# Kernel tuning notes

Hardware: AMD Instinct MI355X
Metric: run time of the kernel (lower is better)

The kernel has to match this reference:

```python
import jax, jax.numpy as jnp
import numpy as np

D = H = W = 128
NUM_STEPS = 7  # MONAI DVF2DDF default


def _base_grid(dtype):
    zz, yy, xx = jnp.meshgrid(jnp.arange(D, dtype=dtype),
                              jnp.arange(H, dtype=dtype),
                              jnp.arange(W, dtype=dtype), indexing='ij')
    return jnp.stack([zz, yy, xx], 0)  # [3,D,H,W] voxel coords


def _warp(img, ddf, mode):
    # img: [1,C,D,H,W], ddf: [1,3,D,H,W] in voxel units.
    # Equivalent to grid_sample(align_corners=True, padding='border'):
    # border padding == clamp the voxel-space sample coordinate to [0, dim-1].
    dtype = ddf.dtype
    coords = _base_grid(dtype) + ddf[0]
    lims = jnp.array([D - 1, H - 1, W - 1], dtype=dtype).reshape(3, 1, 1, 1)
    coords = jnp.clip(coords, 0.0, lims)
    vol = img[0]  # [C,D,H,W]
    if mode == 'nearest':
        zi, yi, xi = jnp.round(coords).astype(jnp.int32)
        return vol[:, zi, yi, xi][None]
    z, y, x = coords
    z0 = jnp.floor(z); y0 = jnp.floor(y); x0 = jnp.floor(x)
    wz = z - z0; wy = y - y0; wx = x - x0
    z0i = z0.astype(jnp.int32); y0i = y0.astype(jnp.int32); x0i = x0.astype(jnp.int32)
    z1i = jnp.minimum(z0i + 1, D - 1)
    y1i = jnp.minimum(y0i + 1, H - 1)
    x1i = jnp.minimum(x0i + 1, W - 1)
    g = lambda a, b, c: vol[:, a, b, c]  # [C,D,H,W] gather
    out = (g(z0i, y0i, x0i) * (1 - wz) * (1 - wy) * (1 - wx)
         + g(z0i, y0i, x1i) * (1 - wz) * (1 - wy) * wx
         + g(z0i, y1i, x0i) * (1 - wz) * wy * (1 - wx)
         + g(z0i, y1i, x1i) * (1 - wz) * wy * wx
         + g(z1i, y0i, x0i) * wz * (1 - wy) * (1 - wx)
         + g(z1i, y0i, x1i) * wz * (1 - wy) * wx
         + g(z1i, y1i, x0i) * wz * wy * (1 - wx)
         + g(z1i, y1i, x1i) * wz * wy * wx)
    return out[None]


def _dvf2ddf(dvf):
    # scaling-and-squaring integration of a stationary velocity field
    ddf = dvf / (2.0 ** NUM_STEPS)
    for _ in range(NUM_STEPS):
        ddf = ddf + _warp(ddf, ddf, 'bilinear')
    return ddf


def setup_inputs() -> dict:
    key = jax.random.key(0)
    k1, k2, k3, k4 = jax.random.split(key, 4)
    dvf = jax.random.normal(k1, (1, 3, D, H, W), dtype=jnp.float32) * 0.5
    moving_image = jax.random.uniform(k2, (1, 1, D, H, W), dtype=jnp.float32)
    fixed_image = jax.random.uniform(k3, (1, 1, D, H, W), dtype=jnp.float32)
    moving_label = jax.random.randint(k4, (1, 1, D, H, W), 0, 4).astype(jnp.float32)
    return {'dvf': dvf, 'moving_image': moving_image,
            'fixed_image': fixed_image, 'moving_label': moving_label}


def reference(dvf, moving_image, fixed_image, moving_label):
    ddf = _dvf2ddf(dvf)
    pred_image = _warp(moving_image, ddf, 'bilinear')
    pred_label = _warp(moving_label, ddf, 'nearest')
    return (ddf, pred_image, pred_label, dvf)
```

## Files before the change

### kernel.cpp

```cpp
#include <hip/hip_runtime.h>

#define DD 128
constexpr int NV = DD * DD * DD;
constexpr float SCALE = 1.0f / 128.0f;

__device__ __forceinline__ float clampc(float v) {
    return fminf(fmaxf(v, 0.0f), (float)(DD - 1));
}

struct Corners {
    int i000, i001, i010, i011, i100, i101, i110, i111;
    float w000, w001, w010, w011, w100, w101, w110, w111;
};

__device__ __forceinline__ Corners corner_setup(float cz, float cy, float cx) {
    float z0f = floorf(cz), y0f = floorf(cy), x0f = floorf(cx);
    float wz = cz - z0f, wy = cy - y0f, wx = cx - x0f;
    int z0 = (int)z0f, y0 = (int)y0f, x0 = (int)x0f;
    int z1 = min(z0 + 1, DD - 1);
    int y1 = min(y0 + 1, DD - 1);
    int x1 = min(x0 + 1, DD - 1);
    float omz = 1.0f - wz, omy = 1.0f - wy, omx = 1.0f - wx;
    int zs0 = z0 << 14, zs1 = z1 << 14;
    int ys0 = y0 << 7,  ys1 = y1 << 7;
    Corners c;
    c.i000 = zs0 + ys0 + x0; c.i001 = zs0 + ys0 + x1;
    c.i010 = zs0 + ys1 + x0; c.i011 = zs0 + ys1 + x1;
    c.i100 = zs1 + ys0 + x0; c.i101 = zs1 + ys0 + x1;
    c.i110 = zs1 + ys1 + x0; c.i111 = zs1 + ys1 + x1;
    c.w000 = omz * omy * omx; c.w001 = omz * omy * wx;
    c.w010 = omz * wy * omx;  c.w011 = omz * wy * wx;
    c.w100 = wz * omy * omx;  c.w101 = wz * omy * wx;
    c.w110 = wz * wy * omx;   c.w111 = wz * wy * wx;
    return c;
}

__device__ __forceinline__ float3 trilerp4(const float4* __restrict__ src,
                                           const Corners& c, float3 base) {
    float4 v000 = src[c.i000], v001 = src[c.i001];
    float4 v010 = src[c.i010], v011 = src[c.i011];
    float4 v100 = src[c.i100], v101 = src[c.i101];
    float4 v110 = src[c.i110], v111 = src[c.i111];
    float3 r;
    r.x = base.x + c.w000*v000.x + c.w001*v001.x + c.w010*v010.x + c.w011*v011.x
                 + c.w100*v100.x + c.w101*v101.x + c.w110*v110.x + c.w111*v111.x;
    r.y = base.y + c.w000*v000.y + c.w001*v001.y + c.w010*v010.y + c.w011*v011.y
                 + c.w100*v100.y + c.w101*v101.y + c.w110*v110.y + c.w111*v111.y;
    r.z = base.z + c.w000*v000.z + c.w001*v001.z + c.w010*v010.z + c.w011*v011.z
                 + c.w100*v100.z + c.w101*v101.z + c.w110*v110.z + c.w111*v111.z;
    return r;
}


__global__ __launch_bounds__(256)
void pack_kernel(const float* __restrict__ dvf, float4* __restrict__ dst) {
    int tid = blockIdx.x * blockDim.x + threadIdx.x;
    float4 v;
    v.x = dvf[tid] * SCALE;
    v.y = dvf[tid + NV] * SCALE;
    v.z = dvf[tid + 2 * NV] * SCALE;
    v.w = 0.0f;
    dst[tid] = v;
}

__global__ __launch_bounds__(256)
void step_pair_kernel(const float4* __restrict__ src, float4* __restrict__ dst) {
    int t = blockIdx.x * blockDim.x + threadIdx.x;
    int x  = t & (DD - 1);
    int y  = (t >> 7) & (DD - 1);
    int zh = t >> 14;
    int z  = zh << 1;

    int idxA = (z << 14) + (y << 7) + x;
    int idxB = idxA + (1 << 14);

    float4 sA = src[idxA];
    float4 sB = src[idxB];

    Corners cA = corner_setup(clampc((float)z + sA.x),
                              clampc((float)y + sA.y),
                              clampc((float)x + sA.z));
    Corners cB = corner_setup(clampc((float)(z + 1) + sB.x),
                              clampc((float)y + sB.y),
                              clampc((float)x + sB.z));

    float3 rA = trilerp4(src, cA, make_float3(sA.x, sA.y, sA.z));
    float3 rB = trilerp4(src, cB, make_float3(sB.x, sB.y, sB.z));

    dst[idxA] = make_float4(rA.x, rA.y, rA.z, 0.0f);
    dst[idxB] = make_float4(rB.x, rB.y, rB.z, 0.0f);
}

__global__ __launch_bounds__(256)
void step7_final4_kernel(const float4* __restrict__ src,
                         const float* __restrict__ mimg,
                         const float* __restrict__ mlab,
                         const float* __restrict__ dvf,
                         float* __restrict__ ddf_out,
                         float* __restrict__ pred_img,
                         float* __restrict__ pred_lab,
                         float* __restrict__ dvf_out) {
    int tid = blockIdx.x * blockDim.x + threadIdx.x;
    int x = tid & (DD - 1);
    int y = (tid >> 7) & (DD - 1);
    int z = tid >> 14;

    float4 s = src[tid];
    float dv0 = dvf[tid], dv1 = dvf[tid + NV], dv2 = dvf[tid + 2 * NV];

    Corners c = corner_setup(clampc((float)z + s.x),
                             clampc((float)y + s.y),
                             clampc((float)x + s.z));
    float3 r = trilerp4(src, c, make_float3(s.x, s.y, s.z));

    ddf_out[tid]          = r.x;
    ddf_out[tid + NV]     = r.y;
    ddf_out[tid + 2 * NV] = r.z;
    dvf_out[tid]          = dv0;
    dvf_out[tid + NV]     = dv1;
    dvf_out[tid + 2 * NV] = dv2;

    float cz = clampc((float)z + r.x);
    float cy = clampc((float)y + r.y);
    float cx = clampc((float)x + r.z);

    {
        Corners g = corner_setup(cz, cy, cx);
        pred_img[tid] = g.w000*mimg[g.i000] + g.w001*mimg[g.i001]
                      + g.w010*mimg[g.i010] + g.w011*mimg[g.i011]
                      + g.w100*mimg[g.i100] + g.w101*mimg[g.i101]
                      + g.w110*mimg[g.i110] + g.w111*mimg[g.i111];
    }
    {
        int zi = (int)rintf(cz);
        int yi = (int)rintf(cy);
        int xi = (int)rintf(cx);
        pred_lab[tid] = mlab[(zi << 14) + (yi << 7) + xi];
    }
}


__device__ __forceinline__ void trilerp3i(const float* __restrict__ src,
                                          const Corners& c,
                                          float& r0, float& r1, float& r2) {
    const float* p000 = src + 3 * c.i000; const float* p001 = src + 3 * c.i001;
    const float* p010 = src + 3 * c.i010; const float* p011 = src + 3 * c.i011;
    const float* p100 = src + 3 * c.i100; const float* p101 = src + 3 * c.i101;
    const float* p110 = src + 3 * c.i110; const float* p111 = src + 3 * c.i111;
    r0 = c.w000*p000[0] + c.w001*p001[0] + c.w010*p010[0] + c.w011*p011[0]
       + c.w100*p100[0] + c.w101*p101[0] + c.w110*p110[0] + c.w111*p111[0];
    r1 = c.w000*p000[1] + c.w001*p001[1] + c.w010*p010[1] + c.w011*p011[1]
       + c.w100*p100[1] + c.w101*p101[1] + c.w110*p110[1] + c.w111*p111[1];
    r2 = c.w000*p000[2] + c.w001*p001[2] + c.w010*p010[2] + c.w011*p011[2]
       + c.w100*p100[2] + c.w101*p101[2] + c.w110*p110[2] + c.w111*p111[2];
}

__global__ __launch_bounds__(256)
void init3_kernel(const float* __restrict__ dvf, float* __restrict__ A) {
    int tid = blockIdx.x * blockDim.x + threadIdx.x;
    float* p = A + 3 * tid;
    p[0] = dvf[tid] * SCALE;
    p[1] = dvf[tid + NV] * SCALE;
    p[2] = dvf[tid + 2 * NV] * SCALE;
}

__global__ __launch_bounds__(256)
void step3_kernel(const float* __restrict__ src, float* __restrict__ dst) {
    int tid = blockIdx.x * blockDim.x + threadIdx.x;
    int x = tid & (DD - 1);
    int y = (tid >> 7) & (DD - 1);
    int z = tid >> 14;
    const float* s = src + 3 * tid;
    float d0 = s[0], d1 = s[1], d2 = s[2];
    Corners c = corner_setup(clampc((float)z + d0),
                             clampc((float)y + d1),
                             clampc((float)x + d2));
    float r0, r1, r2;
    trilerp3i(src, c, r0, r1, r2);
    float* p = dst + 3 * tid;
    p[0] = d0 + r0; p[1] = d1 + r1; p[2] = d2 + r2;
}

__global__ __launch_bounds__(256)
void step7_final3_kernel(const float* __restrict__ src,
                         const float* __restrict__ mimg,
                         const float* __restrict__ mlab,
                         const float* __restrict__ dvf,
                         float* __restrict__ ddf_out,
                         float* __restrict__ pred_img,
                         float* __restrict__ pred_lab,
                         float* __restrict__ dvf_out) {
    int tid = blockIdx.x * blockDim.x + threadIdx.x;
    int x = tid & (DD - 1);
    int y = (tid >> 7) & (DD - 1);
    int z = tid >> 14;
    const float* s = src + 3 * tid;
    float d0 = s[0], d1 = s[1], d2 = s[2];
    Corners c = corner_setup(clampc((float)z + d0),
                             clampc((float)y + d1),
                             clampc((float)x + d2));
    float r0, r1, r2;
    trilerp3i(src, c, r0, r1, r2);
    r0 += d0; r1 += d1; r2 += d2;
    ddf_out[tid]          = r0;
    ddf_out[tid + NV]     = r1;
    ddf_out[tid + 2 * NV] = r2;
    dvf_out[tid]          = dvf[tid];
    dvf_out[tid + NV]     = dvf[tid + NV];
    dvf_out[tid + 2 * NV] = dvf[tid + 2 * NV];
    float cz = clampc((float)z + r0);
    float cy = clampc((float)y + r1);
    float cx = clampc((float)x + r2);
    {
        Corners g = corner_setup(cz, cy, cx);
        pred_img[tid] = g.w000*mimg[g.i000] + g.w001*mimg[g.i001]
                      + g.w010*mimg[g.i010] + g.w011*mimg[g.i011]
                      + g.w100*mimg[g.i100] + g.w101*mimg[g.i101]
                      + g.w110*mimg[g.i110] + g.w111*mimg[g.i111];
    }
    {
        int zi = (int)rintf(cz);
        int yi = (int)rintf(cy);
        int xi = (int)rintf(cx);
        pred_lab[tid] = mlab[(zi << 14) + (yi << 7) + xi];
    }
}


extern "C" void kernel_launch(void* const* d_in, const int* in_sizes, int n_in,
                              void* d_out, int out_size, void* d_ws, size_t ws_size,
                              hipStream_t stream) {
    const float* dvf  = (const float*)d_in[0];
    const float* mimg = (const float*)d_in[1];
    const float* mlab = (const float*)d_in[3];

    float* out      = (float*)d_out;
    float* ddf_out  = out;
    float* pred_img = out + 3 * NV;
    float* pred_lab = out + 4 * NV;
    float* dvf_out  = out + 5 * NV;

    dim3 block(256);
    dim3 grid(NV / 256);
    dim3 gridh(NV / 512);

    if (ws_size >= (size_t)NV * 4 * sizeof(float)) {
        float4* P = (float4*)d_ws;
        float4* Q = (float4*)(out + 4 * NV);

        pack_kernel<<<grid, block, 0, stream>>>(dvf, P);
        step_pair_kernel<<<gridh, block, 0, stream>>>(P, Q);
        step_pair_kernel<<<gridh, block, 0, stream>>>(Q, P);
        step_pair_kernel<<<gridh, block, 0, stream>>>(P, Q);
        step_pair_kernel<<<gridh, block, 0, stream>>>(Q, P);
        step_pair_kernel<<<gridh, block, 0, stream>>>(P, Q);
        step_pair_kernel<<<gridh, block, 0, stream>>>(Q, P);
        step7_final4_kernel<<<grid, block, 0, stream>>>(P, mimg, mlab, dvf,
                                                        ddf_out, pred_img,
                                                        pred_lab, dvf_out);
    } else {
        float* A = dvf_out;
        float* B = ddf_out;
        init3_kernel<<<grid, block, 0, stream>>>(dvf, A);
        step3_kernel<<<grid, block, 0, stream>>>(A, B);
        step3_kernel<<<grid, block, 0, stream>>>(B, A);
        step3_kernel<<<grid, block, 0, stream>>>(A, B);
        step3_kernel<<<grid, block, 0, stream>>>(B, A);
        step3_kernel<<<grid, block, 0, stream>>>(A, B);
        step3_kernel<<<grid, block, 0, stream>>>(B, A);
        step7_final3_kernel<<<grid, block, 0, stream>>>(A, mimg, mlab, dvf,
                                                        ddf_out, pred_img,
                                                        pred_lab, dvf_out);
    }
}
```

Before: 280.2 us.

## Stage displacement tiles with halo in LDS for scaling-and-squaring steps

Replaces the per-thread global gather step kernel with a tiled kernel. Each block loads an 8x8x32 tile plus a 2-voxel halo of the displacement field into shared memory as three planar arrays, then does the trilinear interpolation from LDS, falling back to global gathers when a sample leaves the tile. The aim is to cut redundant global and L2 traffic from the eight-corner gathers. The cost is a cooperative halo load with integer div/mod, a sync, and divergence for out-of-tile samples. Displacements early in the integration are small, but they grow with each squaring step.

```diff
diff --git a/kernel.cpp b/kernel.cpp
--- a/kernel.cpp
+++ b/kernel.cpp
@@ -4,35 +4,57 @@
 constexpr int NV = DD * DD * DD;
 constexpr float SCALE = 1.0f / 128.0f;
 
+#define TZ 8
+#define TY 8
+#define TX 32
+#define HALO 2
+#define SZ (TZ + 2 * HALO)
+#define SY (TY + 2 * HALO)
+#define SX (TX + 2 * HALO)
+#define SVOX (SZ * SY * SX)
+
 __device__ __forceinline__ float clampc(float v) {
     return fminf(fmaxf(v, 0.0f), (float)(DD - 1));
 }
 
-struct Corners {
-    int i000, i001, i010, i011, i100, i101, i110, i111;
+struct CornerC {
+    int z0, z1, y0, y1, x0, x1;
     float w000, w001, w010, w011, w100, w101, w110, w111;
 };
 
-__device__ __forceinline__ Corners corner_setup(float cz, float cy, float cx) {
+__device__ __forceinline__ CornerC corner_setup_c(float cz, float cy, float cx) {
     float z0f = floorf(cz), y0f = floorf(cy), x0f = floorf(cx);
     float wz = cz - z0f, wy = cy - y0f, wx = cx - x0f;
-    int z0 = (int)z0f, y0 = (int)y0f, x0 = (int)x0f;
-    int z1 = min(z0 + 1, DD - 1);
-    int y1 = min(y0 + 1, DD - 1);
-    int x1 = min(x0 + 1, DD - 1);
+    CornerC c;
+    c.z0 = (int)z0f; c.y0 = (int)y0f; c.x0 = (int)x0f;
+    c.z1 = min(c.z0 + 1, DD - 1);
+    c.y1 = min(c.y0 + 1, DD - 1);
+    c.x1 = min(c.x0 + 1, DD - 1);
     float omz = 1.0f - wz, omy = 1.0f - wy, omx = 1.0f - wx;
-    int zs0 = z0 << 14, zs1 = z1 << 14;
-    int ys0 = y0 << 7,  ys1 = y1 << 7;
-    Corners c;
-    c.i000 = zs0 + ys0 + x0; c.i001 = zs0 + ys0 + x1;
-    c.i010 = zs0 + ys1 + x0; c.i011 = zs0 + ys1 + x1;
-    c.i100 = zs1 + ys0 + x0; c.i101 = zs1 + ys0 + x1;
-    c.i110 = zs1 + ys1 + x0; c.i111 = zs1 + ys1 + x1;
     c.w000 = omz * omy * omx; c.w001 = omz * omy * wx;
     c.w010 = omz * wy * omx;  c.w011 = omz * wy * wx;
     c.w100 = wz * omy * omx;  c.w101 = wz * omy * wx;
     c.w110 = wz * wy * omx;   c.w111 = wz * wy * wx;
     return c;
+}
+
+struct Corners {
+    int i000, i001, i010, i011, i100, i101, i110, i111;
+    float w000, w001, w010, w011, w100, w101, w110, w111;
+};
+
+__device__ __forceinline__ Corners corner_setup(float cz, float cy, float cx) {
+    CornerC c = corner_setup_c(cz, cy, cx);
+    Corners g;
+    int zs0 = c.z0 << 14, zs1 = c.z1 << 14;
+    int ys0 = c.y0 << 7,  ys1 = c.y1 << 7;
+    g.i000 = zs0 + ys0 + c.x0; g.i001 = zs0 + ys0 + c.x1;
+    g.i010 = zs0 + ys1 + c.x0; g.i011 = zs0 + ys1 + c.x1;
+    g.i100 = zs1 + ys0 + c.x0; g.i101 = zs1 + ys0 + c.x1;
+    g.i110 = zs1 + ys1 + c.x0; g.i111 = zs1 + ys1 + c.x1;
+    g.w000 = c.w000; g.w001 = c.w001; g.w010 = c.w010; g.w011 = c.w011;
+    g.w100 = c.w100; g.w101 = c.w101; g.w110 = c.w110; g.w111 = c.w111;
+    return g;
 }
 
 __device__ __forceinline__ float3 trilerp4(const float4* __restrict__ src,
@@ -64,31 +86,83 @@
 }
 
 __global__ __launch_bounds__(256)
-void step_pair_kernel(const float4* __restrict__ src, float4* __restrict__ dst) {
-    int t = blockIdx.x * blockDim.x + threadIdx.x;
-    int x  = t & (DD - 1);
-    int y  = (t >> 7) & (DD - 1);
-    int zh = t >> 14;
-    int z  = zh << 1;
-
-    int idxA = (z << 14) + (y << 7) + x;
-    int idxB = idxA + (1 << 14);
-
-    float4 sA = src[idxA];
-    float4 sB = src[idxB];
-
-    Corners cA = corner_setup(clampc((float)z + sA.x),
-                              clampc((float)y + sA.y),
-                              clampc((float)x + sA.z));
-    Corners cB = corner_setup(clampc((float)(z + 1) + sB.x),
-                              clampc((float)y + sB.y),
-                              clampc((float)x + sB.z));
-
-    float3 rA = trilerp4(src, cA, make_float3(sA.x, sA.y, sA.z));
-    float3 rB = trilerp4(src, cB, make_float3(sB.x, sB.y, sB.z));
-
-    dst[idxA] = make_float4(rA.x, rA.y, rA.z, 0.0f);
-    dst[idxB] = make_float4(rB.x, rB.y, rB.z, 0.0f);
+void step_lds_kernel(const float4* __restrict__ src, float4* __restrict__ dst) {
+    __shared__ float sf0[SVOX];
+    __shared__ float sf1[SVOX];
+    __shared__ float sf2[SVOX];
+
+    int bid = blockIdx.x;
+    int X0 = (bid & 3) * TX;
+    int Y0 = ((bid >> 2) & 15) * TY;
+    int Z0 = (bid >> 6) * TZ;
+    int t = threadIdx.x;
+
+    for (int s = t; s < SVOX; s += 256) {
+        int xp = s % SX;
+        int r  = s / SX;
+        int yp = r % SY;
+        int zp = r / SY;
+        int gz = min(max(Z0 - HALO + zp, 0), DD - 1);
+        int gy = min(max(Y0 - HALO + yp, 0), DD - 1);
+        int gx = min(max(X0 - HALO + xp, 0), DD - 1);
+        float4 v = src[(gz << 14) + (gy << 7) + gx];
+        sf0[s] = v.x; sf1[s] = v.y; sf2[s] = v.z;
+    }
+    __syncthreads();
+
+    int tx = t & (TX - 1);
+    int ty = t >> 5;
+    int x = X0 + tx, y = Y0 + ty;
+
+    for (int lz = 0; lz < TZ; ++lz) {
+        int z = Z0 + lz;
+        int sown = ((lz + HALO) * SY + (ty + HALO)) * SX + (tx + HALO);
+        float d0 = sf0[sown], d1 = sf1[sown], d2 = sf2[sown];
+
+        float cz = clampc((float)z + d0);
+        float cy = clampc((float)y + d1);
+        float cx = clampc((float)x + d2);
+        CornerC c = corner_setup_c(cz, cy, cx);
+
+        int lz0 = c.z0 - (Z0 - HALO), lz1 = c.z1 - (Z0 - HALO);
+        int ly0 = c.y0 - (Y0 - HALO), ly1 = c.y1 - (Y0 - HALO);
+        int lx0 = c.x0 - (X0 - HALO), lx1 = c.x1 - (X0 - HALO);
+        bool in_tile = (lz0 >= 0) & (lz1 < SZ) & (ly0 >= 0) & (ly1 < SY)
+                     & (lx0 >= 0) & (lx1 < SX);
+
+        float r0, r1, r2;
+        if (__builtin_expect(in_tile, 1)) {
+            int b00 = (lz0 * SY + ly0) * SX;
+            int b01 = (lz0 * SY + ly1) * SX;
+            int b10 = (lz1 * SY + ly0) * SX;
+            int b11 = (lz1 * SY + ly1) * SX;
+            int a000 = b00 + lx0, a001 = b00 + lx1;
+            int a010 = b01 + lx0, a011 = b01 + lx1;
+            int a100 = b10 + lx0, a101 = b10 + lx1;
+            int a110 = b11 + lx0, a111 = b11 + lx1;
+            r0 = c.w000*sf0[a000] + c.w001*sf0[a001] + c.w010*sf0[a010] + c.w011*sf0[a011]
+               + c.w100*sf0[a100] + c.w101*sf0[a101] + c.w110*sf0[a110] + c.w111*sf0[a111];
+            r1 = c.w000*sf1[a000] + c.w001*sf1[a001] + c.w010*sf1[a010] + c.w011*sf1[a011]
+               + c.w100*sf1[a100] + c.w101*sf1[a101] + c.w110*sf1[a110] + c.w111*sf1[a111];
+            r2 = c.w000*sf2[a000] + c.w001*sf2[a001] + c.w010*sf2[a010] + c.w011*sf2[a011]
+               + c.w100*sf2[a100] + c.w101*sf2[a101] + c.w110*sf2[a110] + c.w111*sf2[a111];
+        } else {
+            int zs0 = c.z0 << 14, zs1 = c.z1 << 14;
+            int ys0 = c.y0 << 7,  ys1 = c.y1 << 7;
+            float4 v000 = src[zs0 + ys0 + c.x0], v001 = src[zs0 + ys0 + c.x1];
+            float4 v010 = src[zs0 + ys1 + c.x0], v011 = src[zs0 + ys1 + c.x1];
+            float4 v100 = src[zs1 + ys0 + c.x0], v101 = src[zs1 + ys0 + c.x1];
+            float4 v110 = src[zs1 + ys1 + c.x0], v111 = src[zs1 + ys1 + c.x1];
+            r0 = c.w000*v000.x + c.w001*v001.x + c.w010*v010.x + c.w011*v011.x
+               + c.w100*v100.x + c.w101*v101.x + c.w110*v110.x + c.w111*v111.x;
+            r1 = c.w000*v000.y + c.w001*v001.y + c.w010*v010.y + c.w011*v011.y
+               + c.w100*v100.y + c.w101*v101.y + c.w110*v110.y + c.w111*v111.y;
+            r2 = c.w000*v000.z + c.w001*v001.z + c.w010*v010.z + c.w011*v011.z
+               + c.w100*v100.z + c.w101*v101.z + c.w110*v110.z + c.w111*v111.z;
+        }
+
+        dst[(z << 14) + (y << 7) + x] = make_float4(d0 + r0, d1 + r1, d2 + r2, 0.0f);
+    }
 }
 
 __global__ __launch_bounds__(256)
@@ -242,19 +316,19 @@
 
     dim3 block(256);
     dim3 grid(NV / 256);
-    dim3 gridh(NV / 512);
+    dim3 gridT(NV / (TZ * TY * TX));
 
     if (ws_size >= (size_t)NV * 4 * sizeof(float)) {
         float4* P = (float4*)d_ws;
         float4* Q = (float4*)(out + 4 * NV);
 
         pack_kernel<<<grid, block, 0, stream>>>(dvf, P);
-        step_pair_kernel<<<gridh, block, 0, stream>>>(P, Q);
-        step_pair_kernel<<<gridh, block, 0, stream>>>(Q, P);
-        step_pair_kernel<<<gridh, block, 0, stream>>>(P, Q);
-        step_pair_kernel<<<gridh, block, 0, stream>>>(Q, P);
-        step_pair_kernel<<<gridh, block, 0, stream>>>(P, Q);
-        step_pair_kernel<<<gridh, block, 0, stream>>>(Q, P);
+        step_lds_kernel<<<gridT, block, 0, stream>>>(P, Q);
+        step_lds_kernel<<<gridT, block, 0, stream>>>(Q, P);
+        step_lds_kernel<<<gridT, block, 0, stream>>>(P, Q);
+        step_lds_kernel<<<gridT, block, 0, stream>>>(Q, P);
+        step_lds_kernel<<<gridT, block, 0, stream>>>(P, Q);
+        step_lds_kernel<<<gridT, block, 0, stream>>>(Q, P);
         step7_final4_kernel<<<grid, block, 0, stream>>>(P, mimg, mlab, dvf,
                                                         ddf_out, pred_img,
                                                         pred_lab, dvf_out);
```

After: 329.5 us. 1.18x slower.
